# Kernel optimization log

Measured on AMD Instinct MI355X. Metric: run time of the kernel, lower is better.

The kernel has to match this reference:

```python
import jax, jax.numpy as jnp
import numpy as np

B, S, D_IN, D_ST = 4, 4096, 1024, 1024


def setup_inputs() -> dict:
    key = jax.random.key(0)
    ks = jax.random.split(key, 7)
    s_in = 1.0 / np.sqrt(D_IN)
    s_st = 1.0 / np.sqrt(D_ST)
    return {
        "x": jax.random.normal(ks[0], (B, S, D_IN), dtype=jnp.float32),
        "gate_w": jax.random.uniform(ks[1], (D_IN, D_ST), jnp.float32, -s_in, s_in),
        "gate_b": jax.random.uniform(ks[2], (D_ST,), jnp.float32, -s_in, s_in),
        "inp_w": jax.random.uniform(ks[3], (D_IN, D_ST), jnp.float32, -s_in, s_in),
        "inp_b": jax.random.uniform(ks[4], (D_ST,), jnp.float32, -s_in, s_in),
        "out_w": jax.random.uniform(ks[5], (D_ST, D_IN), jnp.float32, -s_st, s_st),
        "out_b": jax.random.uniform(ks[6], (D_IN,), jnp.float32, -s_st, s_st),
    }


def reference(x, gate_w, gate_b, inp_w, inp_b, out_w, out_b):
    # x: [B, S, D_in]
    inp = jnp.einsum("bsd,de->bse", x, inp_w) + inp_b      # [B,S,Dst]
    gate = jax.nn.sigmoid(jnp.einsum("bsd,de->bse", x, gate_w) + gate_b)
    b_t = (1.0 - gate) * inp                               # [B,S,Dst]

    # affine recurrence h_t = gate_t * h_{t-1} + b_t via lax.scan over time
    def step(h, ab):
        a, b = ab
        h = a * h + b
        return h, h

    a_sb = jnp.swapaxes(gate, 0, 1)  # [S,B,Dst]
    b_sb = jnp.swapaxes(b_t, 0, 1)
    h0 = jnp.zeros((x.shape[0], inp.shape[-1]), dtype=x.dtype)
    _, hs = jax.lax.scan(step, h0, (a_sb, b_sb))           # [S,B,Dst]
    scan_out = jnp.swapaxes(hs, 0, 1)                      # [B,S,Dst]

    return x + jnp.einsum("bse,ed->bsd", scan_out, out_w) + out_b
```

## Files before the change

### kernel.cpp

```cpp
#include <hip/hip_runtime.h>

typedef unsigned short u16;
typedef unsigned int   u32;
typedef __bf16 bf16x8 __attribute__((ext_vector_type(8)));
typedef float  f32x4  __attribute__((ext_vector_type(4)));

#define DEVI __device__ __forceinline__

DEVI u16 f2bf(float f) {
    union { float f; u32 u; } c; c.f = f;
    u32 u = c.u;
    u32 r = (u + 0x7fffu + ((u >> 16) & 1u)) >> 16;
    return (u16)r;
}
DEVI float bf2f(u16 v) {
    union { u32 u; float f; } c; c.u = ((u32)v) << 16;
    return c.f;
}

DEVI void gload16(const void* g, void* l) {
    __builtin_amdgcn_global_load_lds(
        (const __attribute__((address_space(1))) void*)g,
        (__attribute__((address_space(3))) void*)l, 16, 0, 0);
}


#define VMW(N)  asm volatile("s_waitcnt vmcnt(" #N ")" ::: "memory")
#define LGKM(N) asm volatile("s_waitcnt lgkmcnt(" #N ")" ::: "memory")
#define BAR     __builtin_amdgcn_s_barrier()
#define SP1     __builtin_amdgcn_s_setprio(1)
#define SP0     __builtin_amdgcn_s_setprio(0)
#define SCB     __builtin_amdgcn_sched_barrier(0)

DEVI void stage_half(const u16* g, u16* slot, int tid) {
    const int r = tid >> 3;
    const int ks = ((tid & 7) << 3) ^ (((tid >> 5) & 1) << 4);
    gload16(g + (long)r * 1024 + ks, slot + tid * 8);
    gload16(g + (long)(r + 64) * 1024 + ks, slot + 4096 + tid * 8);
}

DEVI f32x4 mfma(const bf16x8& a, const bf16x8& b, const f32x4& c) {
    return __builtin_amdgcn_mfma_f32_16x16x32_bf16(a, b, c, 0, 0, 0);
}

#define PH(Q, M2, READB, STG, GATE)                                          \
    {                                                                        \
        if (READB) {                                                         \
            _Pragma("unroll")                                                \
            for (int n = 0; n < 4; ++n) {                                    \
                bh[n][0] = *(const bf16x8*)(lds + (Q) + bbase + n * 1024);   \
                bh[n][1] = *(const bf16x8*)(lds + (Q) + bbase + n * 1024 + 32); \
            }                                                                \
        }                                                                    \
        a0k0 = *(const bf16x8*)(lds + (Q) + abase + (M2) * 2048);            \
        a0k1 = *(const bf16x8*)(lds + (Q) + abase + (M2) * 2048 + 32);       \
        a1k0 = *(const bf16x8*)(lds + (Q) + abase + (M2) * 2048 + 1024);     \
        a1k1 = *(const bf16x8*)(lds + (Q) + abase + (M2) * 2048 + 1056);     \
        STG;                                                                 \
        if (READB) { LGKM(8); }                                              \
        BAR;                                                                 \
        LGKM(0); SCB;                                                        \
        SP1;                                                                 \
        _Pragma("unroll")                                                    \
        for (int n = 0; n < 4; ++n) {                                        \
            acc[(M2) * 2][n]     = mfma(a0k0, bh[n][0], acc[(M2) * 2][n]);   \
            acc[(M2) * 2][n]     = mfma(a0k1, bh[n][1], acc[(M2) * 2][n]);   \
            acc[(M2) * 2 + 1][n] = mfma(a1k0, bh[n][0], acc[(M2) * 2 + 1][n]); \
            acc[(M2) * 2 + 1][n] = mfma(a1k1, bh[n][1], acc[(M2) * 2 + 1][n]); \
        }                                                                    \
        SP0;                                                                 \
        GATE;                                                                \
        BAR;                                                                 \
    }

#define NOP do {} while (0)
#define AH(t, h) (Ab + (long)(h) * 131072 + (t) * 64)
#define BH(t, h) (Bb + (long)(h) * 131072 + (t) * 64)

DEVI void pipe256(const u16* Ab, const u16* Bb, u16* lds,
                  f32x4 (&acc)[8][4], int tid) {
    const int lane = tid & 63;
    const int wm = (tid >> 6) >> 2, wn = (tid >> 6) & 3;
    const int kswz = ((lane >> 4) << 3) ^ (((lane >> 2) & 1) << 4);
    const int abase = wm * 8192 + (lane & 15) * 64 + kswz;
    const int bbase = 16384 + (wn >> 1) * 8192 + ((wn & 1) * 64 + (lane & 15)) * 64 + kswz;

    stage_half(AH(0, 0), lds + 0,             tid);
    stage_half(AH(0, 1), lds + 8192,          tid);
    stage_half(BH(0, 0), lds + 16384,         tid);
    stage_half(BH(0, 1), lds + 24576,         tid);
    stage_half(BH(1, 0), lds + 32768 + 16384, tid);
    stage_half(BH(1, 1), lds + 32768 + 24576, tid);
    VMW(4); BAR;

    bf16x8 bh[4][2];
    bf16x8 a0k0, a0k1, a1k0, a1k1;

#pragma unroll 1
    for (int j = 0; j < 7; ++j) {
        const int T = 2 * j;
        PH(0, 0, 1, stage_half(AH(T + 1, 0), lds + 32768, tid), NOP);
        PH(0, 1, 0, stage_half(AH(T + 1, 1), lds + 32768 + 8192, tid), NOP);
        PH(0, 2, 0, stage_half(BH(T + 2, 0), lds + 16384, tid), NOP);
        PH(0, 3, 0, stage_half(BH(T + 2, 1), lds + 24576, tid), VMW(4));
        PH(32768, 0, 1, stage_half(AH(T + 2, 0), lds + 0, tid), NOP);
        PH(32768, 1, 0, stage_half(AH(T + 2, 1), lds + 8192, tid), NOP);
        PH(32768, 2, 0, stage_half(BH(T + 3, 0), lds + 32768 + 16384, tid), NOP);
        PH(32768, 3, 0, stage_half(BH(T + 3, 1), lds + 32768 + 24576, tid), VMW(4));
    }
    PH(0, 0, 1, stage_half(AH(15, 0), lds + 32768, tid), NOP);
    PH(0, 1, 0, stage_half(AH(15, 1), lds + 32768 + 8192, tid), NOP);
    PH(0, 2, 0, NOP, NOP);
    PH(0, 3, 0, NOP, VMW(0));
    PH(32768, 0, 1, NOP, NOP);
    PH(32768, 1, 0, NOP, NOP);
    PH(32768, 2, 0, NOP, NOP);
    PH(32768, 3, 0, NOP, NOP);
}


__global__ __launch_bounds__(512, 1) void k_gemm_cat8(
    const u16* __restrict__ A, const u16* __restrict__ Bcat,
    const float* __restrict__ gb, const float* __restrict__ ib,
    u32* __restrict__ ab) {
    __shared__ __align__(16) u16 lds[65536];
    const int tid = threadIdx.x, lane = tid & 63;
    const int wm = (tid >> 6) >> 2, wn = (tid >> 6) & 3;

    int fid = (int)blockIdx.y * 8 + (int)blockIdx.x;
    int swz = (fid & 7) * 64 + (fid >> 3);
    const long bn = swz & 7, bm = swz >> 3;

    f32x4 acc[8][4] = {};
    pipe256(A + bm * 256 * 1024, Bcat + bn * 256 * 1024, lds, acc, tid);

    const long rbase = bm * 256 + wm * 128;
    const int chbase = (int)bn * 128 + wn * 32;
#pragma unroll
    for (int t = 0; t < 2; ++t) {
        int ch = chbase + t * 16 + (lane & 15);
        float g0 = gb[ch], i0 = ib[ch];
#pragma unroll
        for (int m = 0; m < 8; ++m) {
            long row = rbase + m * 16 + ((lane >> 4) << 2);
#pragma unroll
            for (int i = 0; i < 4; ++i) {
                float pg = acc[m][2 * t][i] + g0;
                float pi = acc[m][2 * t + 1][i] + i0;
                float aa = 1.0f / (1.0f + __expf(-pg));
                float bb = (1.0f - aa) * pi;
                ab[(row + i) * 1024 + ch] = (u32)f2bf(aa) | ((u32)f2bf(bb) << 16);
            }
        }
    }
}


__global__ __launch_bounds__(512, 1) void k_gemm_out8(
    const u16* __restrict__ A, const u16* __restrict__ Bt,
    const u16* __restrict__ xbf, const float* __restrict__ ob,
    float* __restrict__ out) {
    __shared__ __align__(16) u16 lds[65536];
    const int tid = threadIdx.x, lane = tid & 63;
    const int wm = (tid >> 6) >> 2, wn = (tid >> 6) & 3;

    int fid = (int)blockIdx.y * 4 + (int)blockIdx.x;
    int swz = (fid & 7) * 32 + (fid >> 3);
    const long bn = swz & 3, bm = swz >> 2;

    f32x4 acc[8][4] = {};
    pipe256(A + bm * 256 * 1024, Bt + bn * 256 * 1024, lds, acc, tid);

    const long rbase = bm * 256 + wm * 128;
    const int cbase = (int)bn * 256 + wn * 64;
#pragma unroll
    for (int n = 0; n < 4; ++n) {
        int col = cbase + n * 16 + (lane & 15);
        float o0 = ob[col];
#pragma unroll
        for (int m = 0; m < 8; ++m) {
            long row = rbase + m * 16 + ((lane >> 4) << 2);
#pragma unroll
            for (int i = 0; i < 4; ++i) {
                long o = (row + i) * 1024 + col;
                out[o] = acc[m][n][i] + o0 + bf2f(xbf[o]);
            }
        }
    }
}


__global__ __launch_bounds__(256) void k_cvt_x(const float4* __restrict__ x,
                                               uint2* __restrict__ o, int n4) {
    int i = blockIdx.x * 256 + threadIdx.x;
    if (i < n4) {
        float4 v = x[i];
        uint2 r;
        r.x = (u32)f2bf(v.x) | ((u32)f2bf(v.y) << 16);
        r.y = (u32)f2bf(v.z) | ((u32)f2bf(v.w) << 16);
        o[i] = r;
    }
}

__global__ __launch_bounds__(256) void k_transpose_bf(const float* __restrict__ w,
                                                      u16* __restrict__ wt, int R, int C) {
    __shared__ float t[32][33];
    int c0 = blockIdx.x * 32, r0 = blockIdx.y * 32;
    int x = threadIdx.x & 31, y = threadIdx.x >> 5;
    for (int i = y; i < 32; i += 8) t[i][x] = w[(size_t)(r0 + i) * C + c0 + x];
    __syncthreads();
    for (int i = y; i < 32; i += 8) wt[(size_t)(c0 + i) * R + r0 + x] = f2bf(t[x][i]);
}

__global__ __launch_bounds__(256) void k_transpose_cat(const float* __restrict__ gw,
                                                       const float* __restrict__ iw,
                                                       u16* __restrict__ wt, int K, int C) {
    __shared__ float t[32][33];
    int c0 = blockIdx.x * 32, r0 = blockIdx.y * 32;
    const float* w = blockIdx.z ? iw : gw;
    int x = threadIdx.x & 31, y = threadIdx.x >> 5;
    for (int i = y; i < 32; i += 8) t[i][x] = w[(size_t)(r0 + i) * C + c0 + x];
    __syncthreads();
    for (int i = y; i < 32; i += 8) {
        int ch = c0 + i;
        int r = ((ch >> 4) << 5) | ((int)blockIdx.z << 4) | (ch & 15);
        wt[(size_t)r * K + r0 + x] = f2bf(t[x][i]);
    }
}


__global__ __launch_bounds__(256) void k_scanA(const u32* __restrict__ ab,
                                               float2* __restrict__ cAB) {
    int e = blockIdx.x * 256 + threadIdx.x;
    int c = blockIdx.y, bt = blockIdx.z;
    long base = ((long)bt * 4096 + c * 64) * 1024 + e;
    float Aa = 1.f, H = 0.f;
#pragma unroll 4
    for (int i = 0; i < 64; ++i) {
        u32 v = ab[base + (long)i * 1024];
        float a = bf2f((u16)v), b = bf2f((u16)(v >> 16));
        H = a * H + b;
        Aa *= a;
    }
    cAB[((long)bt * 64 + c) * 1024 + e] = make_float2(Aa, H);
}

__global__ __launch_bounds__(256) void k_scanB(const float2* __restrict__ cAB,
                                               float* __restrict__ hin) {
    int e = blockIdx.x * 256 + threadIdx.x;
    int bt = blockIdx.y;
    float H = 0.f;
#pragma unroll
    for (int c = 0; c < 64; ++c) {
        long s = ((long)bt * 64 + c) * 1024 + e;
        hin[s] = H;
        float2 v = cAB[s];
        H = v.x * H + v.y;
    }
}

__global__ __launch_bounds__(256) void k_scanC(const u32* __restrict__ ab,
                                               const float* __restrict__ hin,
                                               u16* __restrict__ hout) {
    int e = blockIdx.x * 256 + threadIdx.x;
    int c = blockIdx.y, bt = blockIdx.z;
    long base = ((long)bt * 4096 + c * 64) * 1024 + e;
    float H = hin[((long)bt * 64 + c) * 1024 + e];
#pragma unroll 4
    for (int i = 0; i < 64; ++i) {
        u32 v = ab[base + (long)i * 1024];
        H = bf2f((u16)v) * H + bf2f((u16)(v >> 16));
        hout[base + (long)i * 1024] = f2bf(H);
    }
}


extern "C" void kernel_launch(void* const* d_in, const int* in_sizes, int n_in,
                              void* d_out, int out_size, void* d_ws, size_t ws_size,
                              hipStream_t stream) {
    const float* x      = (const float*)d_in[0];
    const float* gate_w = (const float*)d_in[1];
    const float* gate_b = (const float*)d_in[2];
    const float* inp_w  = (const float*)d_in[3];
    const float* inp_b  = (const float*)d_in[4];
    const float* out_w  = (const float*)d_in[5];
    const float* out_b  = (const float*)d_in[6];
    float* out = (float*)d_out;

    const int Bsz = 4, S = 4096, Din = 1024, Dst = 1024;
    const int M = Bsz * S;
    const long nx = (long)M * Din;

    char* w = (char*)d_ws;
    u16* xb      = (u16*)(w);
    u16* catW    = (u16*)(w + 33554432);
    u16* owT     = (u16*)(w + 37748736);
    u16* hbf     = (u16*)(w + 39845888);
    float2* cAB  = (float2*)(w + 73400320);
    float* hin   = (float*)(w + 75497472);

    u32* ab = (u32*)d_out;

    k_cvt_x<<<(int)(nx / 4 / 256), 256, 0, stream>>>((const float4*)x, (uint2*)xb, (int)(nx / 4));
    k_transpose_cat<<<dim3(Dst / 32, Din / 32, 2), 256, 0, stream>>>(gate_w, inp_w, catW, Din, Dst);
    k_transpose_bf<<<dim3(Din / 32, Dst / 32), 256, 0, stream>>>(out_w, owT, Dst, Din);

    k_gemm_cat8<<<dim3(8, M / 256), 512, 0, stream>>>(xb, catW, gate_b, inp_b, ab);

    k_scanA<<<dim3(4, 64, Bsz), 256, 0, stream>>>(ab, cAB);
    k_scanB<<<dim3(4, Bsz), 256, 0, stream>>>(cAB, hin);
    k_scanC<<<dim3(4, 64, Bsz), 256, 0, stream>>>(ab, hin, hbf);

    k_gemm_out8<<<dim3(4, M / 256), 512, 0, stream>>>(hbf, owT, xb, out_b, out);
}
```

Measured before the change: 190.5 us.

## Fuse scan chunk-summary into gate GEMM epilogue and merge prep kernels

The gate/input GEMM epilogue now computes per-64-row chunk affine summaries (product of a, accumulated b) from its register tile, using lane shuffles across the four row groups. This removes the separate scanA pass, which re-read the whole 128 MB ab buffer. The x conversion and the two weight transposes are also merged into one launch to cut launch overhead. The cost is extra shuffles and serial arithmetic in the GEMM epilogue, and the chunk summaries now rely on the GEMM tile mapping lining up with the 64-row chunks.

```diff
diff --git a/kernel.cpp b/kernel.cpp
--- a/kernel.cpp
+++ b/kernel.cpp
@@ -122,7 +122,7 @@
 __global__ __launch_bounds__(512, 1) void k_gemm_cat8(
     const u16* __restrict__ A, const u16* __restrict__ Bcat,
     const float* __restrict__ gb, const float* __restrict__ ib,
-    u32* __restrict__ ab) {
+    u32* __restrict__ ab, float2* __restrict__ cAB) {
     __shared__ __align__(16) u16 lds[65536];
     const int tid = threadIdx.x, lane = tid & 63;
     const int wm = (tid >> 6) >> 2, wn = (tid >> 6) & 3;
@@ -136,6 +136,7 @@
 
     const long rbase = bm * 256 + wm * 128;
     const int chbase = (int)bn * 128 + wn * 32;
+    float sA[2][8], sB[2][8];
 #pragma unroll
     for (int t = 0; t < 2; ++t) {
         int ch = chbase + t * 16 + (lane & 15);
@@ -143,13 +144,43 @@
 #pragma unroll
         for (int m = 0; m < 8; ++m) {
             long row = rbase + m * 16 + ((lane >> 4) << 2);
+            float Aseg = 1.0f, Bseg = 0.0f;
 #pragma unroll
             for (int i = 0; i < 4; ++i) {
                 float pg = acc[m][2 * t][i] + g0;
                 float pi = acc[m][2 * t + 1][i] + i0;
                 float aa = 1.0f / (1.0f + __expf(-pg));
                 float bb = (1.0f - aa) * pi;
-                ab[(row + i) * 1024 + ch] = (u32)f2bf(aa) | ((u32)f2bf(bb) << 16);
+                u16 au = f2bf(aa), bu = f2bf(bb);
+                ab[(row + i) * 1024 + ch] = (u32)au | ((u32)bu << 16);
+                float ar = bf2f(au), br = bf2f(bu);
+                Aseg = ar * Aseg;
+                Bseg = ar * Bseg + br;
+            }
+            sA[t][m] = Aseg;
+            sB[t][m] = Bseg;
+        }
+    }
+#pragma unroll
+    for (int t = 0; t < 2; ++t) {
+#pragma unroll
+        for (int c2 = 0; c2 < 2; ++c2) {
+            float Ac = 1.0f, Bc = 0.0f;
+#pragma unroll
+            for (int mm = 0; mm < 4; ++mm) {
+                int m = c2 * 4 + mm;
+#pragma unroll
+                for (int q = 0; q < 4; ++q) {
+                    float Aq = __shfl(sA[t][m], (lane & 15) + q * 16);
+                    float Bq = __shfl(sB[t][m], (lane & 15) + q * 16);
+                    Ac = Aq * Ac;
+                    Bc = Aq * Bc + Bq;
+                }
+            }
+            if ((lane >> 4) == 0) {
+                long gc = (rbase >> 6) + c2;
+                int ch = chbase + t * 16 + (lane & 15);
+                cAB[gc * 1024 + ch] = make_float2(Ac, Bc);
             }
         }
     }
@@ -190,60 +221,44 @@
 }
 
 
-__global__ __launch_bounds__(256) void k_cvt_x(const float4* __restrict__ x,
-                                               uint2* __restrict__ o, int n4) {
-    int i = blockIdx.x * 256 + threadIdx.x;
-    if (i < n4) {
-        float4 v = x[i];
+__global__ __launch_bounds__(256) void k_prep(
+    const float4* __restrict__ x4, uint2* __restrict__ xb2,
+    const float* __restrict__ gw, const float* __restrict__ iw,
+    u16* __restrict__ catW, const float* __restrict__ ow,
+    u16* __restrict__ owT) {
+    __shared__ float t[32][33];
+    int bid = blockIdx.x;
+    if (bid < 16384) {
+        int i = bid * 256 + threadIdx.x;
+        float4 v = x4[i];
         uint2 r;
         r.x = (u32)f2bf(v.x) | ((u32)f2bf(v.y) << 16);
         r.y = (u32)f2bf(v.z) | ((u32)f2bf(v.w) << 16);
-        o[i] = r;
-    }
-}
-
-__global__ __launch_bounds__(256) void k_transpose_bf(const float* __restrict__ w,
-                                                      u16* __restrict__ wt, int R, int C) {
-    __shared__ float t[32][33];
-    int c0 = blockIdx.x * 32, r0 = blockIdx.y * 32;
-    int x = threadIdx.x & 31, y = threadIdx.x >> 5;
-    for (int i = y; i < 32; i += 8) t[i][x] = w[(size_t)(r0 + i) * C + c0 + x];
-    __syncthreads();
-    for (int i = y; i < 32; i += 8) wt[(size_t)(c0 + i) * R + r0 + x] = f2bf(t[x][i]);
-}
-
-__global__ __launch_bounds__(256) void k_transpose_cat(const float* __restrict__ gw,
-                                                       const float* __restrict__ iw,
-                                                       u16* __restrict__ wt, int K, int C) {
-    __shared__ float t[32][33];
-    int c0 = blockIdx.x * 32, r0 = blockIdx.y * 32;
-    const float* w = blockIdx.z ? iw : gw;
-    int x = threadIdx.x & 31, y = threadIdx.x >> 5;
-    for (int i = y; i < 32; i += 8) t[i][x] = w[(size_t)(r0 + i) * C + c0 + x];
-    __syncthreads();
-    for (int i = y; i < 32; i += 8) {
-        int ch = c0 + i;
-        int r = ((ch >> 4) << 5) | ((int)blockIdx.z << 4) | (ch & 15);
-        wt[(size_t)r * K + r0 + x] = f2bf(t[x][i]);
-    }
-}
-
-
-__global__ __launch_bounds__(256) void k_scanA(const u32* __restrict__ ab,
-                                               float2* __restrict__ cAB) {
-    int e = blockIdx.x * 256 + threadIdx.x;
-    int c = blockIdx.y, bt = blockIdx.z;
-    long base = ((long)bt * 4096 + c * 64) * 1024 + e;
-    float Aa = 1.f, H = 0.f;
-#pragma unroll 4
-    for (int i = 0; i < 64; ++i) {
-        u32 v = ab[base + (long)i * 1024];
-        float a = bf2f((u16)v), b = bf2f((u16)(v >> 16));
-        H = a * H + b;
-        Aa *= a;
-    }
-    cAB[((long)bt * 64 + c) * 1024 + e] = make_float2(Aa, H);
-}
+        xb2[i] = r;
+        return;
+    }
+    int xi = threadIdx.x & 31, y = threadIdx.x >> 5;
+    if (bid < 18432) {
+        int q = bid - 16384;
+        int c0 = (q & 31) * 32, r0 = ((q >> 5) & 31) * 32, z = q >> 10;
+        const float* w = z ? iw : gw;
+        for (int i = y; i < 32; i += 8) t[i][xi] = w[(size_t)(r0 + i) * 1024 + c0 + xi];
+        __syncthreads();
+        for (int i = y; i < 32; i += 8) {
+            int ch = c0 + i;
+            int r = ((ch >> 4) << 5) | (z << 4) | (ch & 15);
+            catW[(size_t)r * 1024 + r0 + xi] = f2bf(t[xi][i]);
+        }
+    } else {
+        int q = bid - 18432;
+        int c0 = (q & 31) * 32, r0 = (q >> 5) * 32;
+        for (int i = y; i < 32; i += 8) t[i][xi] = ow[(size_t)(r0 + i) * 1024 + c0 + xi];
+        __syncthreads();
+        for (int i = y; i < 32; i += 8)
+            owT[(size_t)(c0 + i) * 1024 + r0 + xi] = f2bf(t[xi][i]);
+    }
+}
+
 
 __global__ __launch_bounds__(256) void k_scanB(const float2* __restrict__ cAB,
                                                float* __restrict__ hin) {
@@ -289,7 +304,6 @@
 
     const int Bsz = 4, S = 4096, Din = 1024, Dst = 1024;
     const int M = Bsz * S;
-    const long nx = (long)M * Din;
 
     char* w = (char*)d_ws;
     u16* xb      = (u16*)(w);
@@ -301,13 +315,11 @@
 
     u32* ab = (u32*)d_out;
 
-    k_cvt_x<<<(int)(nx / 4 / 256), 256, 0, stream>>>((const float4*)x, (uint2*)xb, (int)(nx / 4));
-    k_transpose_cat<<<dim3(Dst / 32, Din / 32, 2), 256, 0, stream>>>(gate_w, inp_w, catW, Din, Dst);
-    k_transpose_bf<<<dim3(Din / 32, Dst / 32), 256, 0, stream>>>(out_w, owT, Dst, Din);
-
-    k_gemm_cat8<<<dim3(8, M / 256), 512, 0, stream>>>(xb, catW, gate_b, inp_b, ab);
-
-    k_scanA<<<dim3(4, 64, Bsz), 256, 0, stream>>>(ab, cAB);
+    k_prep<<<19456, 256, 0, stream>>>((const float4*)x, (uint2*)xb,
+                                      gate_w, inp_w, catW, out_w, owT);
+
+    k_gemm_cat8<<<dim3(8, M / 256), 512, 0, stream>>>(xb, catW, gate_b, inp_b, ab, cAB);
+
     k_scanB<<<dim3(4, Bsz), 256, 0, stream>>>(cAB, hin);
     k_scanC<<<dim3(4, 64, Bsz), 256, 0, stream>>>(ab, hin, hbf);
 
```

After: 175.8 us. 1.08x faster.
